# Performance work log

Hardware: AMD Instinct MI355X
Metric: run time of the kernel (lower is better)

The kernel has to match this reference:

```python
import jax, jax.numpy as jnp
import numpy as np

INPUT_SIZE = 4
HIDDEN = 2048
OUTPUT_SIZE = 2
NOISE_STD = 0.05
ALPHA = 0.2
RANK = 2
N_SUPPORTS = 2
GDIM = 2 * RANK + INPUT_SIZE  # gaussian_basis_dim default
BATCH = 32
SEQ = 1000


def setup_inputs() -> dict:
    key = jax.random.key(0)
    ks = jax.random.split(key, 8)
    inp = jax.random.normal(ks[0], (BATCH, SEQ, INPUT_SIZE), dtype=jnp.float32)
    noise = jax.random.normal(ks[1], (BATCH, SEQ, HIDDEN), dtype=jnp.float32)
    gaussian_basis = jax.random.normal(ks[2], (GDIM, HIDDEN), dtype=jnp.float32)
    # supports: block indicator masks over hidden units (equal split, weights=None)
    sup = np.zeros((N_SUPPORTS, HIDDEN), dtype=np.float32)
    l = HIDDEN // N_SUPPORTS
    for i in range(N_SUPPORTS):
        sup[i, l * i:l * (i + 1)] = 1.0
    supports = jnp.asarray(sup)
    wi_weights = jax.random.normal(ks[3], (INPUT_SIZE, N_SUPPORTS, GDIM), dtype=jnp.float32)
    m_weights = jax.random.normal(ks[4], (RANK, N_SUPPORTS, GDIM), dtype=jnp.float32) / jnp.sqrt(jnp.float32(HIDDEN))
    n_weights = jax.random.normal(ks[5], (RANK, N_SUPPORTS, GDIM), dtype=jnp.float32) / jnp.sqrt(jnp.float32(HIDDEN))
    wo_weights = jax.random.normal(ks[6], (OUTPUT_SIZE, N_SUPPORTS, GDIM), dtype=jnp.float32) / jnp.float32(HIDDEN)
    wi_biases = jnp.zeros((INPUT_SIZE, N_SUPPORTS), dtype=jnp.float32)
    m_biases = jnp.zeros((RANK, N_SUPPORTS), dtype=jnp.float32)
    n_biases = jnp.zeros((RANK, N_SUPPORTS), dtype=jnp.float32)
    h0_weights = jnp.zeros((N_SUPPORTS, GDIM), dtype=jnp.float32)
    return {
        "input": inp, "noise": noise,
        "wi_weights": wi_weights, "m_weights": m_weights, "n_weights": n_weights,
        "wo_weights": wo_weights, "wi_biases": wi_biases, "m_biases": m_biases,
        "n_biases": n_biases, "h0_weights": h0_weights,
        "gaussian_basis": gaussian_basis, "supports": supports,
    }


def _proxy_params(wi_weights, m_weights, n_weights, wo_weights,
                  wi_biases, m_biases, n_biases, h0_weights,
                  gaussian_basis, supports):
    # (X, S, G) @ (G, H) -> (X, S, H); mask by supports (S, H); sum over S
    def mix(w):
        return jnp.einsum('xsg,gh->xsh', w, gaussian_basis)
    wi = jnp.sum(mix(wi_weights) * supports, axis=1) + wi_biases @ supports      # (I, H)
    m = (jnp.sum(mix(m_weights) * supports, axis=1) + m_biases @ supports).T     # (H, R)
    n = (jnp.sum(mix(n_weights) * supports, axis=1) + n_biases @ supports).T     # (H, R)
    wo = jnp.sum(mix(wo_weights) * supports, axis=1).T                            # (H, O)
    h0 = jnp.sum((h0_weights @ gaussian_basis) * supports, axis=0)                # (H,)
    return wi, m, n, wo, h0


def reference(input, noise, wi_weights, m_weights, n_weights, wo_weights,
              wi_biases, m_biases, n_biases, h0_weights, gaussian_basis, supports):
    wi, m, n, wo, h0 = _proxy_params(wi_weights, m_weights, n_weights, wo_weights,
                                     wi_biases, m_biases, n_biases, h0_weights,
                                     gaussian_basis, supports)
    B = input.shape[0]
    # Precompute external input projection for all steps: (B, T, H)
    xin = jnp.einsum('bti,ih->bth', input, wi)
    h_init = jnp.broadcast_to(h0, (B, h0.shape[0]))
    r_init = jnp.tanh(h_init)

    noise_T = jnp.swapaxes(noise, 0, 1)  # (T, B, H)
    xin_T = jnp.swapaxes(xin, 0, 1)      # (T, B, H)

    def step(carry, xs):
        h, r = carry
        noise_t, xin_t = xs
        h = h + NOISE_STD * noise_t + ALPHA * (-h + (r @ n) @ m.T + xin_t)
        r = jnp.tanh(h)
        return (h, r), r

    _, rs = jax.lax.scan(step, (h_init, r_init), (noise_T, xin_T))  # rs: (T, B, H)
    output = jnp.einsum('tbh,ho->bto', rs, wo)  # (B, T, O)
    return output
```

## Files before the change

### kernel.cpp

```cpp
#include <hip/hip_runtime.h>

#define BATCH 32
#define SEQT 1000
#define INSZ 4
#define HID 2048
#define NOISE_STD 0.05f
#define ALPHA 0.2f
#define ONE_M_ALPHA (1.0f - ALPHA)

#define NTHREADS 512
#define EPT 4
#define NWAVES 8
#define PF 4

template<int CTRL>
__device__ __forceinline__ float dpp_add(float x) {
    int s = __builtin_amdgcn_update_dpp(0, __float_as_int(x), CTRL, 0xF, 0xF, true);
    return x + __int_as_float(s);
}

__device__ __forceinline__ float wave_sum64_to_lane63(float x) {
    x = dpp_add<0x111>(x);
    x = dpp_add<0x112>(x);
    x = dpp_add<0x114>(x);
    x = dpp_add<0x118>(x);
    x = dpp_add<0x142>(x);
    x = dpp_add<0x143>(x);
    return x;
}

__device__ __forceinline__ float sum8_to_lane7(float x) {
    x = dpp_add<0x111>(x);
    x = dpp_add<0x112>(x);
    x = dpp_add<0x114>(x);
    return x;
}

__device__ __forceinline__ float read_lane(float x, int l) {
    return __int_as_float(__builtin_amdgcn_readlane(__float_as_int(x), l));
}

__device__ __forceinline__ float fast_tanh(float x) {
    float e = __expf(2.0f * x);
    return 1.0f - 2.0f * __builtin_amdgcn_rcpf(e + 1.0f);
}

#define LDS_BARRIER() __asm__ volatile("s_waitcnt lgkmcnt(0)\ns_barrier" ::: "memory")

__global__ __launch_bounds__(NTHREADS)
void rnn_kernel(const float* __restrict__ input,
                const float* __restrict__ noise,
                const float* __restrict__ wi_w,
                const float* __restrict__ m_w,
                const float* __restrict__ n_w,
                const float* __restrict__ wo_w,
                const float* __restrict__ wi_b,
                const float* __restrict__ m_b,
                const float* __restrict__ n_b,
                const float* __restrict__ h0_w,
                const float* __restrict__ gb,
                const float* __restrict__ sup,
                float* __restrict__ out)
{
    __shared__ float4 sIn4[SEQT];
    __shared__ float4 sRed[2][NWAVES];

    const int b    = blockIdx.x;
    const int tid  = threadIdx.x;
    const int wave = tid >> 6;
    const int lane = tid & 63;

    const float4* inRow4 = reinterpret_cast<const float4*>(input + (size_t)b * SEQT * INSZ);
    for (int i = tid; i < SEQT; i += NTHREADS)
        sIn4[i] = inRow4[i];

    const int hbase = tid * EPT;
    float wiA[INSZ][EPT];
    float mA0[EPT], mA1[EPT];
    float n0P[EPT], n1P[EPT], wo0P[EPT], wo1P[EPT];
    float hP[EPT];

    float p0 = 0.f, p1 = 0.f, p2 = 0.f, p3 = 0.f;

    #pragma unroll
    for (int e = 0; e < EPT; ++e) {
        const int h = hbase + e;
        float gv[8];
        #pragma unroll
        for (int g = 0; g < 8; ++g) gv[g] = gb[g * HID + h];
        const float s0 = sup[h];
        const float s1 = sup[HID + h];

        auto mix = [&](const float* w) -> float {
            float a0 = 0.f, a1 = 0.f;
            #pragma unroll
            for (int g = 0; g < 8; ++g) { a0 += w[g] * gv[g]; a1 += w[8 + g] * gv[g]; }
            return s0 * a0 + s1 * a1;
        };

        #pragma unroll
        for (int i = 0; i < INSZ; ++i)
            wiA[i][e] = ALPHA * (mix(wi_w + i * 16) + wi_b[i * 2 + 0] * s0 + wi_b[i * 2 + 1] * s1);
        mA0[e]  = ALPHA * (mix(m_w)      + m_b[0] * s0 + m_b[1] * s1);
        mA1[e]  = ALPHA * (mix(m_w + 16) + m_b[2] * s0 + m_b[3] * s1);
        n0P[e]  = mix(n_w)      + n_b[0] * s0 + n_b[1] * s1;
        n1P[e]  = mix(n_w + 16) + n_b[2] * s0 + n_b[3] * s1;
        wo0P[e] = mix(wo_w);
        wo1P[e] = mix(wo_w + 16);
        {
            float a0 = 0.f, a1 = 0.f;
            #pragma unroll
            for (int g = 0; g < 8; ++g) { a0 += h0_w[g] * gv[g]; a1 += h0_w[8 + g] * gv[g]; }
            const float h0v = s0 * a0 + s1 * a1;
            hP[e] = h0v;
            const float r = fast_tanh(h0v);
            p0 += r * n0P[e];  p1 += r * n1P[e];
            p2 += r * wo0P[e]; p3 += r * wo1P[e];
        }
    }

    const float4* nP = reinterpret_cast<const float4*>(noise + (size_t)b * SEQT * HID)
                       + (hbase >> 2);
    const int rowStride = HID / 4;
    float4 nsA = nP[0];
    float4 nsB = nP[1 * rowStride];
    float4 nsC = nP[2 * rowStride];
    float4 nsD = nP[3 * rowStride];

    float* outRow = out + (size_t)b * SEQT * 2;

    __syncthreads();

    auto do_step = [&](int t, float4& nbuf) {
        float w0 = wave_sum64_to_lane63(p0);
        float w1 = wave_sum64_to_lane63(p1);
        float w2 = wave_sum64_to_lane63(p2);
        float w3 = wave_sum64_to_lane63(p3);
        const int par = t & 1;
        if (lane == 63) sRed[par][wave] = make_float4(w0, w1, w2, w3);

        const float4 nv4 = nbuf;
        const int tpre = (t + PF < SEQT) ? (t + PF) : (SEQT - 1);
        nbuf = nP[(size_t)tpre * rowStride];
        const float4 inv = sIn4[t];
        float acc[EPT];
        const float nv[4] = {nv4.x, nv4.y, nv4.z, nv4.w};
        #pragma unroll
        for (int e = 0; e < EPT; ++e) {
            float xin = wiA[0][e] * inv.x;
            xin = fmaf(wiA[1][e], inv.y, xin);
            xin = fmaf(wiA[2][e], inv.z, xin);
            xin = fmaf(wiA[3][e], inv.w, xin);
            acc[e] = fmaf(hP[e], ONE_M_ALPHA, fmaf(NOISE_STD, nv[e], xin));
        }

        LDS_BARRIER();

        const float4 pr = sRed[par][lane & 7];
        float y0 = sum8_to_lane7(pr.x);
        float y1 = sum8_to_lane7(pr.y);
        y0 = read_lane(y0, 7);
        y1 = read_lane(y1, 7);
        if (t > 0 && wave == 0) {
            float o0 = sum8_to_lane7(pr.z);
            float o1 = sum8_to_lane7(pr.w);
            const float o0v = read_lane(o0, 7);
            const float o1v = read_lane(o1, 7);
            if (lane == 0) {
                float2 ov; ov.x = o0v; ov.y = o1v;
                *reinterpret_cast<float2*>(outRow + (t - 1) * 2) = ov;
            }
        }

        p0 = p1 = p2 = p3 = 0.f;
        #pragma unroll
        for (int e = 0; e < EPT; ++e) {
            float h = fmaf(mA1[e], y1, acc[e]);
            h = fmaf(mA0[e], y0, h);
            hP[e] = h;
            const float r = fast_tanh(h);
            p0 = fmaf(r, n0P[e], p0);  p1 = fmaf(r, n1P[e], p1);
            p2 = fmaf(r, wo0P[e], p2); p3 = fmaf(r, wo1P[e], p3);
        }
    };

    for (int t = 0; t < SEQT; t += PF) {
        do_step(t,     nsA);
        do_step(t + 1, nsB);
        do_step(t + 2, nsC);
        do_step(t + 3, nsD);
    }

    {
        float w2 = wave_sum64_to_lane63(p2);
        float w3 = wave_sum64_to_lane63(p3);
        if (lane == 63) sRed[0][wave] = make_float4(w2, w3, 0.f, 0.f);
        LDS_BARRIER();
        if (wave == 0) {
            const float4 pr = sRed[0][lane & 7];
            float o0 = sum8_to_lane7(pr.x);
            float o1 = sum8_to_lane7(pr.y);
            const float o0v = read_lane(o0, 7);
            const float o1v = read_lane(o1, 7);
            if (lane == 0) {
                float2 ov; ov.x = o0v; ov.y = o1v;
                *reinterpret_cast<float2*>(outRow + (SEQT - 1) * 2) = ov;
            }
        }
    }
}

extern "C" void kernel_launch(void* const* d_in, const int* in_sizes, int n_in,
                              void* d_out, int out_size, void* d_ws, size_t ws_size,
                              hipStream_t stream) {
    const float* input = (const float*)d_in[0];
    const float* noise = (const float*)d_in[1];
    const float* wi_w  = (const float*)d_in[2];
    const float* m_w   = (const float*)d_in[3];
    const float* n_w   = (const float*)d_in[4];
    const float* wo_w  = (const float*)d_in[5];
    const float* wi_b  = (const float*)d_in[6];
    const float* m_b   = (const float*)d_in[7];
    const float* n_b   = (const float*)d_in[8];
    const float* h0_w  = (const float*)d_in[9];
    const float* gb    = (const float*)d_in[10];
    const float* sup   = (const float*)d_in[11];
    float* out = (float*)d_out;

    rnn_kernel<<<dim3(BATCH), dim3(NTHREADS), 0, stream>>>(
        input, noise, wi_w, m_w, n_w, wo_w, wi_b, m_b, n_b, h0_w, gb, sup, out);
}
```

Baseline: 895.0 us.

## Halve block to 4 waves with 8 elements per thread and simpler cross-wave reduction

Each block now runs 256 threads that own 8 hidden units each, split across the two halves of the hidden dimension so noise loads stay coalesced. With 4 waves, the cross-wave reduction becomes two broadcast float4 LDS reads plus scalar adds, replacing the DPP sum and readlane. The barrier is moved before the xin/noise accumulation, and the input row is also prefetched into registers. This shortens the per-step serial barrier and reduction path, at the cost of more ALU work and registers per thread and a shallower noise prefetch depth (2 instead of 4).

Result: slower. 946.2 us (+5.7%).

```diff
diff --git a/kernel.cpp b/kernel.cpp
--- a/kernel.cpp
+++ b/kernel.cpp
@@ -8,10 +8,11 @@
 #define ALPHA 0.2f
 #define ONE_M_ALPHA (1.0f - ALPHA)
 
-#define NTHREADS 512
-#define EPT 4
-#define NWAVES 8
-#define PF 4
+#define NTHREADS 256
+#define NWAVES 4
+#define EPT 8
+#define HALFH 1024
+#define PF 2
 
 template<int CTRL>
 __device__ __forceinline__ float dpp_add(float x) {
@@ -27,17 +28,6 @@
     x = dpp_add<0x142>(x);
     x = dpp_add<0x143>(x);
     return x;
-}
-
-__device__ __forceinline__ float sum8_to_lane7(float x) {
-    x = dpp_add<0x111>(x);
-    x = dpp_add<0x112>(x);
-    x = dpp_add<0x114>(x);
-    return x;
-}
-
-__device__ __forceinline__ float read_lane(float x, int l) {
-    return __int_as_float(__builtin_amdgcn_readlane(__float_as_int(x), l));
 }
 
 __device__ __forceinline__ float fast_tanh(float x) {
@@ -63,7 +53,8 @@
                 float* __restrict__ out)
 {
     __shared__ float4 sIn4[SEQT];
-    __shared__ float4 sRed[2][NWAVES];
+    __shared__ __align__(16) float2 sRedY[2][NWAVES];
+    __shared__ __align__(16) float2 sRedO[2][NWAVES];
 
     const int b    = blockIdx.x;
     const int tid  = threadIdx.x;
@@ -74,17 +65,15 @@
     for (int i = tid; i < SEQT; i += NTHREADS)
         sIn4[i] = inRow4[i];
 
-    const int hbase = tid * EPT;
     float wiA[INSZ][EPT];
     float mA0[EPT], mA1[EPT];
     float n0P[EPT], n1P[EPT], wo0P[EPT], wo1P[EPT];
     float hP[EPT];
-
     float p0 = 0.f, p1 = 0.f, p2 = 0.f, p3 = 0.f;
 
     #pragma unroll
     for (int e = 0; e < EPT; ++e) {
-        const int h = hbase + e;
+        const int h = (e < 4) ? (tid * 4 + e) : (HALFH + tid * 4 + (e - 4));
         float gv[8];
         #pragma unroll
         for (int g = 0; g < 8; ++g) gv[g] = gb[g * HID + h];
@@ -119,32 +108,43 @@
         }
     }
 
-    const float4* nP = reinterpret_cast<const float4*>(noise + (size_t)b * SEQT * HID)
-                       + (hbase >> 2);
+    const float4* nP4 = reinterpret_cast<const float4*>(noise + (size_t)b * SEQT * HID);
     const int rowStride = HID / 4;
-    float4 nsA = nP[0];
-    float4 nsB = nP[1 * rowStride];
-    float4 nsC = nP[2 * rowStride];
-    float4 nsD = nP[3 * rowStride];
+    float4 nsA0 = nP4[0 * rowStride + tid];
+    float4 nsA1 = nP4[0 * rowStride + 256 + tid];
+    float4 nsB0 = nP4[1 * rowStride + tid];
+    float4 nsB1 = nP4[1 * rowStride + 256 + tid];
 
     float* outRow = out + (size_t)b * SEQT * 2;
 
     __syncthreads();
-
-    auto do_step = [&](int t, float4& nbuf) {
+    float4 invA = sIn4[0];
+    float4 invB = sIn4[1];
+
+    auto do_step = [&](int t, float4& nb0, float4& nb1, float4& invReg) {
+        const int par = t & 1;
         float w0 = wave_sum64_to_lane63(p0);
         float w1 = wave_sum64_to_lane63(p1);
+        if (lane == 63) sRedY[par][wave] = make_float2(w0, w1);
         float w2 = wave_sum64_to_lane63(p2);
         float w3 = wave_sum64_to_lane63(p3);
-        const int par = t & 1;
-        if (lane == 63) sRed[par][wave] = make_float4(w0, w1, w2, w3);
-
-        const float4 nv4 = nbuf;
+        if (lane == 63) sRedO[par][wave] = make_float2(w2, w3);
+
+        const float4 na = nb0, nbv = nb1;
+        const float4 inv = invReg;
         const int tpre = (t + PF < SEQT) ? (t + PF) : (SEQT - 1);
-        nbuf = nP[(size_t)tpre * rowStride];
-        const float4 inv = sIn4[t];
+        nb0 = nP4[(size_t)tpre * rowStride + tid];
+        nb1 = nP4[(size_t)tpre * rowStride + 256 + tid];
+        invReg = sIn4[tpre];
+
+        LDS_BARRIER();
+
+        const float4* yv4 = reinterpret_cast<const float4*>(&sRedY[par][0]);
+        const float4 ya = yv4[0];
+        const float4 yb = yv4[1];
+
         float acc[EPT];
-        const float nv[4] = {nv4.x, nv4.y, nv4.z, nv4.w};
+        const float nv[EPT] = {na.x, na.y, na.z, na.w, nbv.x, nbv.y, nbv.z, nbv.w};
         #pragma unroll
         for (int e = 0; e < EPT; ++e) {
             float xin = wiA[0][e] * inv.x;
@@ -154,20 +154,17 @@
             acc[e] = fmaf(hP[e], ONE_M_ALPHA, fmaf(NOISE_STD, nv[e], xin));
         }
 
-        LDS_BARRIER();
-
-        const float4 pr = sRed[par][lane & 7];
-        float y0 = sum8_to_lane7(pr.x);
-        float y1 = sum8_to_lane7(pr.y);
-        y0 = read_lane(y0, 7);
-        y1 = read_lane(y1, 7);
-        if (t > 0 && wave == 0) {
-            float o0 = sum8_to_lane7(pr.z);
-            float o1 = sum8_to_lane7(pr.w);
-            const float o0v = read_lane(o0, 7);
-            const float o1v = read_lane(o1, 7);
+        const float y0 = (ya.x + ya.z) + (yb.x + yb.z);
+        const float y1 = (ya.y + ya.w) + (yb.y + yb.w);
+
+        if (wave == 0 && t > 0) {
+            const float4* ov4 = reinterpret_cast<const float4*>(&sRedO[par][0]);
+            const float4 oa = ov4[0];
+            const float4 ob = ov4[1];
             if (lane == 0) {
-                float2 ov; ov.x = o0v; ov.y = o1v;
+                float2 ov;
+                ov.x = (oa.x + oa.z) + (ob.x + ob.z);
+                ov.y = (oa.y + oa.w) + (ob.y + ob.w);
                 *reinterpret_cast<float2*>(outRow + (t - 1) * 2) = ov;
             }
         }
@@ -185,27 +182,23 @@
     };
 
     for (int t = 0; t < SEQT; t += PF) {
-        do_step(t,     nsA);
-        do_step(t + 1, nsB);
-        do_step(t + 2, nsC);
-        do_step(t + 3, nsD);
+        do_step(t,     nsA0, nsA1, invA);
+        do_step(t + 1, nsB0, nsB1, invB);
     }
 
     {
         float w2 = wave_sum64_to_lane63(p2);
         float w3 = wave_sum64_to_lane63(p3);
-        if (lane == 63) sRed[0][wave] = make_float4(w2, w3, 0.f, 0.f);
+        if (lane == 63) sRedO[0][wave] = make_float2(w2, w3);
         LDS_BARRIER();
-        if (wave == 0) {
-            const float4 pr = sRed[0][lane & 7];
-            float o0 = sum8_to_lane7(pr.x);
-            float o1 = sum8_to_lane7(pr.y);
-            const float o0v = read_lane(o0, 7);
-            const float o1v = read_lane(o1, 7);
-            if (lane == 0) {
-                float2 ov; ov.x = o0v; ov.y = o1v;
-                *reinterpret_cast<float2*>(outRow + (SEQT - 1) * 2) = ov;
-            }
+        if (wave == 0 && lane == 0) {
+            const float4* ov4 = reinterpret_cast<const float4*>(&sRedO[0][0]);
+            const float4 oa = ov4[0];
+            const float4 ob = ov4[1];
+            float2 ov;
+            ov.x = (oa.x + oa.z) + (ob.x + ob.z);
+            ov.y = (oa.y + oa.w) + (ob.y + ob.w);
+            *reinterpret_cast<float2*>(outRow + (SEQT - 1) * 2) = ov;
         }
     }
 }
```

## Pack per-step math into float2 vectors and shorten the critical path after the barrier

Applied to the files above, without the earlier changes.

Per-step elementwise arithmetic now uses two-wide float vectors, so the compiler can emit packed FP32 FMA instructions. The step also reorders its work: the barrier comes right after the reduction store, and the noise and input-row prefetch plus the xin accumulation are placed between the barrier and the use of the reduced values. Input rows are prefetched into registers PF steps ahead instead of being read from LDS each step. Output writes rotate across waves and store directly from lane 7, which removes two readlanes per step from wave 0. The risks are more register pressure and a different schedule around the single per-step barrier.

New measurement: 877.4 us. -2.0%, faster.

```diff
diff --git a/kernel.cpp b/kernel.cpp
--- a/kernel.cpp
+++ b/kernel.cpp
@@ -9,9 +9,13 @@
 #define ONE_M_ALPHA (1.0f - ALPHA)
 
 #define NTHREADS 512
+#define NWAVES 8
 #define EPT 4
-#define NWAVES 8
 #define PF 4
+
+typedef float v2f __attribute__((ext_vector_type(2)));
+
+__device__ __forceinline__ v2f vfma(v2f a, v2f b, v2f c) { return a * b + c; }
 
 template<int CTRL>
 __device__ __forceinline__ float dpp_add(float x) {
@@ -36,8 +40,8 @@
     return x;
 }
 
-__device__ __forceinline__ float read_lane(float x, int l) {
-    return __int_as_float(__builtin_amdgcn_readlane(__float_as_int(x), l));
+__device__ __forceinline__ float read_lane7(float x) {
+    return __int_as_float(__builtin_amdgcn_readlane(__float_as_int(x), 7));
 }
 
 __device__ __forceinline__ float fast_tanh(float x) {
@@ -63,7 +67,7 @@
                 float* __restrict__ out)
 {
     __shared__ float4 sIn4[SEQT];
-    __shared__ float4 sRed[2][NWAVES];
+    __shared__ __align__(16) float4 sRed[2][NWAVES];
 
     const int b    = blockIdx.x;
     const int tid  = threadIdx.x;
@@ -74,17 +78,14 @@
     for (int i = tid; i < SEQT; i += NTHREADS)
         sIn4[i] = inRow4[i];
 
-    const int hbase = tid * EPT;
-    float wiA[INSZ][EPT];
-    float mA0[EPT], mA1[EPT];
-    float n0P[EPT], n1P[EPT], wo0P[EPT], wo1P[EPT];
-    float hP[EPT];
-
-    float p0 = 0.f, p1 = 0.f, p2 = 0.f, p3 = 0.f;
+    v2f wiA[INSZ][2];
+    v2f mA0v[2], mA1v[2], n0v[2], n1v[2], wo0v[2], wo1v[2], hv[2];
+    v2f q0 = {0.f, 0.f}, q1 = q0, q2 = q0, q3 = q0;
 
     #pragma unroll
     for (int e = 0; e < EPT; ++e) {
-        const int h = hbase + e;
+        const int h = tid * 4 + e;
+        const int pi = e >> 1, pc = e & 1;
         float gv[8];
         #pragma unroll
         for (int g = 0; g < 8; ++g) gv[g] = gb[g * HID + h];
@@ -100,112 +101,113 @@
 
         #pragma unroll
         for (int i = 0; i < INSZ; ++i)
-            wiA[i][e] = ALPHA * (mix(wi_w + i * 16) + wi_b[i * 2 + 0] * s0 + wi_b[i * 2 + 1] * s1);
-        mA0[e]  = ALPHA * (mix(m_w)      + m_b[0] * s0 + m_b[1] * s1);
-        mA1[e]  = ALPHA * (mix(m_w + 16) + m_b[2] * s0 + m_b[3] * s1);
-        n0P[e]  = mix(n_w)      + n_b[0] * s0 + n_b[1] * s1;
-        n1P[e]  = mix(n_w + 16) + n_b[2] * s0 + n_b[3] * s1;
-        wo0P[e] = mix(wo_w);
-        wo1P[e] = mix(wo_w + 16);
+            wiA[i][pi][pc] = ALPHA * (mix(wi_w + i * 16) + wi_b[i * 2 + 0] * s0 + wi_b[i * 2 + 1] * s1);
+        mA0v[pi][pc] = ALPHA * (mix(m_w)      + m_b[0] * s0 + m_b[1] * s1);
+        mA1v[pi][pc] = ALPHA * (mix(m_w + 16) + m_b[2] * s0 + m_b[3] * s1);
+        const float n0 = mix(n_w)      + n_b[0] * s0 + n_b[1] * s1;
+        const float n1 = mix(n_w + 16) + n_b[2] * s0 + n_b[3] * s1;
+        const float w0 = mix(wo_w);
+        const float w1 = mix(wo_w + 16);
+        n0v[pi][pc] = n0;  n1v[pi][pc] = n1;
+        wo0v[pi][pc] = w0; wo1v[pi][pc] = w1;
         {
             float a0 = 0.f, a1 = 0.f;
             #pragma unroll
             for (int g = 0; g < 8; ++g) { a0 += h0_w[g] * gv[g]; a1 += h0_w[8 + g] * gv[g]; }
             const float h0v = s0 * a0 + s1 * a1;
-            hP[e] = h0v;
+            hv[pi][pc] = h0v;
             const float r = fast_tanh(h0v);
-            p0 += r * n0P[e];  p1 += r * n1P[e];
-            p2 += r * wo0P[e]; p3 += r * wo1P[e];
+            q0[pc] += r * n0;  q1[pc] += r * n1;
+            q2[pc] += r * w0;  q3[pc] += r * w1;
         }
     }
 
-    const float4* nP = reinterpret_cast<const float4*>(noise + (size_t)b * SEQT * HID)
-                       + (hbase >> 2);
+    const float4* nP4 = reinterpret_cast<const float4*>(noise + (size_t)b * SEQT * HID);
     const int rowStride = HID / 4;
-    float4 nsA = nP[0];
-    float4 nsB = nP[1 * rowStride];
-    float4 nsC = nP[2 * rowStride];
-    float4 nsD = nP[3 * rowStride];
+    float4 nb0 = nP4[0 * rowStride + tid];
+    float4 nb1 = nP4[1 * rowStride + tid];
+    float4 nb2 = nP4[2 * rowStride + tid];
+    float4 nb3 = nP4[3 * rowStride + tid];
 
     float* outRow = out + (size_t)b * SEQT * 2;
 
     __syncthreads();
-
-    auto do_step = [&](int t, float4& nbuf) {
-        float w0 = wave_sum64_to_lane63(p0);
-        float w1 = wave_sum64_to_lane63(p1);
-        float w2 = wave_sum64_to_lane63(p2);
-        float w3 = wave_sum64_to_lane63(p3);
+    float4 inv0 = sIn4[0];
+    float4 inv1 = sIn4[1];
+    float4 inv2 = sIn4[2];
+    float4 inv3 = sIn4[3];
+
+    auto do_step = [&](int t, float4& nbuf, float4& invReg) {
         const int par = t & 1;
+        const float p0 = q0.x + q0.y, p1 = q1.x + q1.y;
+        const float p2 = q2.x + q2.y, p3 = q3.x + q3.y;
+        const float w0 = wave_sum64_to_lane63(p0);
+        const float w1 = wave_sum64_to_lane63(p1);
+        const float w2 = wave_sum64_to_lane63(p2);
+        const float w3 = wave_sum64_to_lane63(p3);
         if (lane == 63) sRed[par][wave] = make_float4(w0, w1, w2, w3);
 
+        LDS_BARRIER();
+
+        const float4 pr = sRed[par][lane & 7];
+        const int tpre = (t + PF < SEQT) ? (t + PF) : (SEQT - 1);
         const float4 nv4 = nbuf;
-        const int tpre = (t + PF < SEQT) ? (t + PF) : (SEQT - 1);
-        nbuf = nP[(size_t)tpre * rowStride];
-        const float4 inv = sIn4[t];
-        float acc[EPT];
-        const float nv[4] = {nv4.x, nv4.y, nv4.z, nv4.w};
-        #pragma unroll
-        for (int e = 0; e < EPT; ++e) {
-            float xin = wiA[0][e] * inv.x;
-            xin = fmaf(wiA[1][e], inv.y, xin);
-            xin = fmaf(wiA[2][e], inv.z, xin);
-            xin = fmaf(wiA[3][e], inv.w, xin);
-            acc[e] = fmaf(hP[e], ONE_M_ALPHA, fmaf(NOISE_STD, nv[e], xin));
+        nbuf = nP4[(size_t)tpre * rowStride + tid];
+        const float4 inv = invReg;
+        invReg = sIn4[tpre];
+
+        const v2f nlo = {nv4.x, nv4.y}, nhi = {nv4.z, nv4.w};
+        v2f acc0 = wiA[0][0] * inv.x;
+        v2f acc1 = wiA[0][1] * inv.x;
+        acc0 = vfma(wiA[1][0], inv.y, acc0);  acc1 = vfma(wiA[1][1], inv.y, acc1);
+        acc0 = vfma(wiA[2][0], inv.z, acc0);  acc1 = vfma(wiA[2][1], inv.z, acc1);
+        acc0 = vfma(wiA[3][0], inv.w, acc0);  acc1 = vfma(wiA[3][1], inv.w, acc1);
+        acc0 = acc0 + nlo * NOISE_STD;        acc1 = acc1 + nhi * NOISE_STD;
+        acc0 = vfma(hv[0], ONE_M_ALPHA, acc0); acc1 = vfma(hv[1], ONE_M_ALPHA, acc1);
+
+        const float y0 = read_lane7(sum8_to_lane7(pr.x));
+        const float y1 = read_lane7(sum8_to_lane7(pr.y));
+
+        if (t > 0 && wave == (t & 7)) {
+            const float oz = sum8_to_lane7(pr.z);
+            const float ow = sum8_to_lane7(pr.w);
+            if (lane == 7)
+                *reinterpret_cast<float2*>(outRow + (t - 1) * 2) = make_float2(oz, ow);
         }
 
-        LDS_BARRIER();
-
-        const float4 pr = sRed[par][lane & 7];
-        float y0 = sum8_to_lane7(pr.x);
-        float y1 = sum8_to_lane7(pr.y);
-        y0 = read_lane(y0, 7);
-        y1 = read_lane(y1, 7);
-        if (t > 0 && wave == 0) {
-            float o0 = sum8_to_lane7(pr.z);
-            float o1 = sum8_to_lane7(pr.w);
-            const float o0v = read_lane(o0, 7);
-            const float o1v = read_lane(o1, 7);
-            if (lane == 0) {
-                float2 ov; ov.x = o0v; ov.y = o1v;
-                *reinterpret_cast<float2*>(outRow + (t - 1) * 2) = ov;
-            }
-        }
-
-        p0 = p1 = p2 = p3 = 0.f;
-        #pragma unroll
-        for (int e = 0; e < EPT; ++e) {
-            float h = fmaf(mA1[e], y1, acc[e]);
-            h = fmaf(mA0[e], y0, h);
-            hP[e] = h;
-            const float r = fast_tanh(h);
-            p0 = fmaf(r, n0P[e], p0);  p1 = fmaf(r, n1P[e], p1);
-            p2 = fmaf(r, wo0P[e], p2); p3 = fmaf(r, wo1P[e], p3);
-        }
+        v2f h2a = vfma(mA1v[0], y1, acc0);
+        v2f h2b = vfma(mA1v[1], y1, acc1);
+        h2a = vfma(mA0v[0], y0, h2a);
+        h2b = vfma(mA0v[1], y0, h2b);
+        hv[0] = h2a; hv[1] = h2b;
+        v2f r2a, r2b;
+        r2a.x = fast_tanh(h2a.x); r2a.y = fast_tanh(h2a.y);
+        r2b.x = fast_tanh(h2b.x); r2b.y = fast_tanh(h2b.y);
+        q0 = r2a * n0v[0];  q0 = vfma(r2b, n0v[1], q0);
+        q1 = r2a * n1v[0];  q1 = vfma(r2b, n1v[1], q1);
+        q2 = r2a * wo0v[0]; q2 = vfma(r2b, wo0v[1], q2);
+        q3 = r2a * wo1v[0]; q3 = vfma(r2b, wo1v[1], q3);
     };
 
     for (int t = 0; t < SEQT; t += PF) {
-        do_step(t,     nsA);
-        do_step(t + 1, nsB);
-        do_step(t + 2, nsC);
-        do_step(t + 3, nsD);
+        do_step(t,     nb0, inv0);
+        do_step(t + 1, nb1, inv1);
+        do_step(t + 2, nb2, inv2);
+        do_step(t + 3, nb3, inv3);
     }
 
     {
-        float w2 = wave_sum64_to_lane63(p2);
-        float w3 = wave_sum64_to_lane63(p3);
+        const float p2 = q2.x + q2.y, p3 = q3.x + q3.y;
+        const float w2 = wave_sum64_to_lane63(p2);
+        const float w3 = wave_sum64_to_lane63(p3);
         if (lane == 63) sRed[0][wave] = make_float4(w2, w3, 0.f, 0.f);
         LDS_BARRIER();
         if (wave == 0) {
             const float4 pr = sRed[0][lane & 7];
-            float o0 = sum8_to_lane7(pr.x);
-            float o1 = sum8_to_lane7(pr.y);
-            const float o0v = read_lane(o0, 7);
-            const float o1v = read_lane(o1, 7);
-            if (lane == 0) {
-                float2 ov; ov.x = o0v; ov.y = o1v;
-                *reinterpret_cast<float2*>(outRow + (SEQT - 1) * 2) = ov;
-            }
+            const float oz = sum8_to_lane7(pr.x);
+            const float ow = sum8_to_lane7(pr.y);
+            if (lane == 7)
+                *reinterpret_cast<float2*>(outRow + (SEQT - 1) * 2) = make_float2(oz, ow);
         }
     }
 }
```
